# Kernel optimization log

Measured on AMD Instinct MI355X. Metric: run time of the kernel, lower is better.

Reference implementation:

```python
import jax, jax.numpy as jnp
import numpy as np

HID_GNN = 64
HID_LSTM = 128
FUTURE = 24
N_HYDRO = 32
N_METEO = 64
B, T, E = 32, 168, 384
SLOPE = 0.01  # F.leaky_relu default


def setup_inputs() -> dict:
    key = jax.random.key(0)
    ks = jax.random.split(key, 12)
    N = N_HYDRO + N_METEO
    data_meteo = jax.random.normal(ks[0], (B, T, N_METEO, 1), jnp.float32)
    data_hydro = jax.random.normal(ks[1], (B, T, N_HYDRO, 1), jnp.float32)
    edge_index = jax.random.randint(ks[2], (2, E), 0, N, dtype=jnp.int64)
    # GraphConv(1, HID_GNN): out = lin_root(x) + lin_rel(sum_j x_j) + bias
    W_root = jax.random.normal(ks[3], (HID_GNN, 1), jnp.float32) * 1.0
    W_rel = jax.random.normal(ks[4], (HID_GNN, 1), jnp.float32) * 1.0
    b_gnn = jnp.zeros((HID_GNN,), jnp.float32)
    # Per-station LSTM weights (torch gate order i,f,g,o), stacked over stations
    sih = 1.0 / np.sqrt(HID_GNN)
    shh = 1.0 / np.sqrt(HID_LSTM)
    Wih = jax.random.normal(ks[5], (N_HYDRO, 4 * HID_LSTM, HID_GNN), jnp.float32) * sih
    Whh = jax.random.normal(ks[6], (N_HYDRO, 4 * HID_LSTM, HID_LSTM), jnp.float32) * shh
    bih = jnp.zeros((N_HYDRO, 4 * HID_LSTM), jnp.float32)
    bhh = jnp.zeros((N_HYDRO, 4 * HID_LSTM), jnp.float32)
    W_lin = jax.random.normal(ks[7], (FUTURE, HID_LSTM), jnp.float32) * shh
    b_lin = jnp.zeros((FUTURE,), jnp.float32)
    return {"data_meteo": data_meteo, "data_hydro": data_hydro, "edge_index": edge_index,
            "W_root": W_root, "W_rel": W_rel, "b_gnn": b_gnn,
            "Wih": Wih, "Whh": Whh, "bih": bih, "bhh": bhh,
            "W_lin": W_lin, "b_lin": b_lin}


def _lstm_last(xs, Wih_s, Whh_s, b_s):
    # xs: [B,T,D]; one station's LSTM; returns last hidden [B,H]
    H = Whh_s.shape[1]
    h0 = jnp.zeros((xs.shape[0], H), xs.dtype)

    def step(carry, xt):
        h, c = carry
        gates = xt @ Wih_s.T + h @ Whh_s.T + b_s  # [B,4H]
        i, f, g, o = jnp.split(gates, 4, axis=-1)
        c = jax.nn.sigmoid(f) * c + jax.nn.sigmoid(i) * jnp.tanh(g)
        h = jax.nn.sigmoid(o) * jnp.tanh(c)
        return (h, c), None

    (hT, _), _ = jax.lax.scan(step, (h0, h0), jnp.swapaxes(xs, 0, 1))
    return hT


def reference(data_meteo, data_hydro, edge_index, W_root, W_rel, b_gnn,
              Wih, Whh, bih, bhh, W_lin, b_lin):
    Bn, Tn, Nh, F = data_hydro.shape
    Nm = data_meteo.shape[2]
    N = Nh + Nm
    # [B,T,N,1] -> one graph per (b,t); same edge_index in every graph
    x = jnp.concatenate([data_hydro, data_meteo], axis=2).reshape(Bn * Tn, N, F)
    src, dst = edge_index[0], edge_index[1]
    agg = jnp.zeros_like(x).at[:, dst].add(x[:, src])  # sum aggregation
    h = x @ W_root.T + agg @ W_rel.T + b_gnn          # GraphConv, [G,N,HID_GNN]
    h = jax.nn.leaky_relu(h, SLOPE)
    hydro = h.reshape(Bn, Tn, N, -1)[:, :, :Nh, :]    # [B,T,Nh,HID_GNN]
    # per-station LSTM: vmap over station axis with station-specific weights
    last = jax.vmap(_lstm_last, in_axes=(2, 0, 0, 0))(hydro, Wih, Whh, bih + bhh)  # [Nh,B,H]
    pred = last @ W_lin.T + b_lin                     # [Nh,B,FUTURE]
    pred = jnp.swapaxes(pred, 0, 1)                   # [B,Nh,FUTURE]
    return jax.nn.leaky_relu(pred, SLOPE)
```

## Files before the change

### kernel.cpp

```cpp
#include <hip/hip_runtime.h>

typedef unsigned short u16;
typedef unsigned int u32;
typedef __attribute__((ext_vector_type(8))) short short8;
typedef __attribute__((ext_vector_type(4))) float floatx4;
typedef __attribute__((ext_vector_type(4))) float float4v;

#define B_ 32
#define T_ 168
#define NH_ 32
#define NM_ 64
#define E_ 384
#define HL_ 128
#define FUT_ 24
#define SLOPE_ 0.01f
#define XP_ 80
#define HP_ 144
#define WIH_LP 72
#define WHH_LP 136
#define OVL_E (T_ * 4 * XP_)
#define XG_B 68
#define XG_T (4 * XG_B)
#define XG_W (4 * XG_T)

#define NS1_ (-1.4426950408889634f)
#define S2_ (2.8853900817779268f)

static __device__ __forceinline__ float b2f(u16 u) {
  u32 v = ((u32)u) << 16;
  return __builtin_bit_cast(float, v);
}
static __device__ __forceinline__ u16 f2bf(float f) {
  u32 x = __builtin_bit_cast(u32, f);
  u32 r = (x + 0x7fffu + ((x >> 16) & 1u)) >> 16;
  return (u16)r;
}
static __device__ __forceinline__ float fexp2(float x) { return __builtin_amdgcn_exp2f(x); }
static __device__ __forceinline__ float frcp(float x) { return __builtin_amdgcn_rcpf(x); }
static __device__ __forceinline__ float sel4(floatx4 v, int r) {
  float m0 = (r & 1) ? v[1] : v[0];
  float m1 = (r & 1) ? v[3] : v[2];
  return (r & 2) ? m1 : m0;
}
static __device__ __forceinline__ float lrelu(float x) { return fmaxf(x, SLOPE_ * x); }

__launch_bounds__(512, 2)
__global__ void fused_kernel(const float* __restrict__ dm, const float* __restrict__ dh,
                             const int* __restrict__ eidx,
                             const float* __restrict__ Wroot, const float* __restrict__ Wrel,
                             const float* __restrict__ bgnn,
                             const float* __restrict__ Wih, const float* __restrict__ Whh,
                             const float* __restrict__ bih, const float* __restrict__ bhh,
                             const float* __restrict__ Wlin, const float* __restrict__ blin,
                             float* __restrict__ out) {
  const int s = blockIdx.x & 31;
  const int bg = blockIdx.x >> 5;
  const int tid = threadIdx.x;
  const int w = tid >> 6;
  const int lane = tid & 63;
  const int cm = lane & 15;
  const int q = lane >> 4;
  const int b = cm & 3;
  const int rho = cm >> 2;

  __shared__ __align__(16) u16 ovl[OVL_E];
  __shared__ __align__(16) u16 hbuf[2 * 4 * HP_];
  __shared__ __align__(16) float xgbuf[8 * XG_W];
  __shared__ float xh_lds[4][T_];
  __shared__ float ag_lds[4][T_];
  __shared__ float wr_s[64], wv_s[64], bg_s[64];
  __shared__ int srcs[E_];
  __shared__ int nsrc, iflag;

  if (tid == 0) { nsrc = 0; iflag = 0; }
  for (int i = tid; i < 2 * 4 * HP_; i += 512) hbuf[i] = 0;
  __syncthreads();

  {
    int odd = 0;
    for (int e = tid; e < E_; e += 512) odd |= eidx[2 * e + 1];
    if (odd) atomicOr(&iflag, 1);
  }
  __syncthreads();
  const bool i32 = iflag != 0;

  for (int e = tid; e < E_; e += 512) {
    int se = i32 ? eidx[e] : eidx[2 * e];
    int de = i32 ? eidx[E_ + e] : eidx[2 * E_ + 2 * e];
    if (de == s) { int i = atomicAdd(&nsrc, 1); srcs[i] = se; }
  }
  if (tid < 64) { wr_s[tid] = Wroot[tid]; wv_s[tid] = Wrel[tid]; bg_s[tid] = bgnn[tid]; }
  for (int i = tid; i < 4 * T_; i += 512) {
    int bb = i / T_, t = i % T_;
    xh_lds[bb][t] = dh[((size_t)(bg * 4 + bb) * T_ + t) * NH_ + s];
  }
  floatx4 bias_init[4];
#pragma unroll
  for (int blk = 0; blk < 4; blk++) {
    const float scb = (blk == 2) ? S2_ : NS1_;
#pragma unroll
    for (int r = 0; r < 4; r++) {
      const int nb = blk * 128 + w * 16 + q * 4 + r;
      bias_init[blk][r] = (bih[s * 512 + nb] + bhh[s * 512 + nb]) * scb;
    }
  }
  __syncthreads();

  const int ns = nsrc;
  for (int i = tid; i < 4 * T_; i += 512) {
    int bb = i / T_, t = i % T_;
    size_t gb = (size_t)(bg * 4 + bb) * T_ + t;
    float a = 0.f;
    for (int j = 0; j < ns; j++) {
      int sr = srcs[j];
      a += (sr < NH_) ? dh[gb * NH_ + sr] : dm[gb * NM_ + (sr - NH_)];
    }
    ag_lds[bb][t] = a;
  }

  short8 Af[4][6];
  const int nl = w * 16 + cm;
  __syncthreads();
  {
    const float* g = Wih + (size_t)s * 512 * 64;
#pragma unroll
    for (int it = 0; it < 16; it++) {
      int j = tid + it * 512;
      float4v v = *(const float4v*)(g + 4 * j);
      const float sc = ((j >> 11) == 2) ? S2_ : NS1_;
      u16* dst = ovl + (j >> 4) * WIH_LP + (j & 15) * 4;
      dst[0] = f2bf(v[0] * sc); dst[1] = f2bf(v[1] * sc);
      dst[2] = f2bf(v[2] * sc); dst[3] = f2bf(v[3] * sc);
    }
  }
  __syncthreads();
#pragma unroll
  for (int blk = 0; blk < 4; blk++)
#pragma unroll
    for (int kk = 0; kk < 2; kk++)
      Af[blk][kk] = *(const short8*)(ovl + (blk * 128 + nl) * WIH_LP + kk * 32 + q * 8);
  __syncthreads();
  {
    const float* g = Whh + (size_t)s * 512 * 128;
#pragma unroll
    for (int it = 0; it < 16; it++) {
      int j = tid + it * 512;
      float4v v = *(const float4v*)(g + 4 * j);
      u16* dst = ovl + (j >> 5) * WHH_LP + (j & 31) * 4;
      dst[0] = f2bf(v[0] * NS1_); dst[1] = f2bf(v[1] * NS1_);
      dst[2] = f2bf(v[2] * NS1_); dst[3] = f2bf(v[3] * NS1_);
    }
  }
  __syncthreads();
#pragma unroll
  for (int blk = 0; blk < 2; blk++)
#pragma unroll
    for (int kk = 0; kk < 4; kk++)
      Af[blk][2 + kk] = *(const short8*)(ovl + (blk * 128 + nl) * WHH_LP + kk * 32 + q * 8);
  __syncthreads();
  {
    const float* g = Whh + ((size_t)s * 512 + 256) * 128;
#pragma unroll
    for (int it = 0; it < 16; it++) {
      int j = tid + it * 512;
      float4v v = *(const float4v*)(g + 4 * j);
      const float sc = (j < 4096) ? S2_ : NS1_;
      u16* dst = ovl + (j >> 5) * WHH_LP + (j & 31) * 4;
      dst[0] = f2bf(v[0] * sc); dst[1] = f2bf(v[1] * sc);
      dst[2] = f2bf(v[2] * sc); dst[3] = f2bf(v[3] * sc);
    }
  }
  __syncthreads();
#pragma unroll
  for (int blk = 2; blk < 4; blk++)
#pragma unroll
    for (int kk = 0; kk < 4; kk++)
      Af[blk][2 + kk] = *(const short8*)(ovl + ((blk - 2) * 128 + nl) * WHH_LP + kk * 32 + q * 8);
  __syncthreads();

  {
    const int k = tid & 63;
    const int bb = (tid >> 6) & 3;
    const int th = tid >> 8;
    const float wrk = wr_s[k], wvk = wv_s[k], bgk = bg_s[k];
    for (int i = 0; i < T_ / 2; i++) {
      const int t = th * (T_ / 2) + i;
      const float xv = xh_lds[bb][t] * wrk + ag_lds[bb][t] * wvk + bgk;
      ovl[t * (4 * XP_) + bb * XP_ + k] = f2bf(lrelu(xv));
    }
  }
  __syncthreads();

  floatx4 zvec;
  zvec[0] = 0.f; zvec[1] = 0.f; zvec[2] = 0.f; zvec[3] = 0.f;
  float* const xgw = xgbuf + w * XG_W + rho * XG_T + b * XG_B + q * 16;
  const float* const xgr = xgbuf + w * XG_W + b * XG_B + q * 16 + rho * 4;

  float c = 0.0f;
  for (int tt = 0; tt < T_ / 4; tt++) {
    {
      const int tb = tt * 4 + rho;
      short8 Bx0 = *(const short8*)(ovl + tb * (4 * XP_) + b * XP_ + q * 8);
      short8 Bx1 = *(const short8*)(ovl + tb * (4 * XP_) + b * XP_ + 32 + q * 8);
      floatx4 ax[4];
#pragma unroll
      for (int blk = 0; blk < 4; blk++) {
        ax[blk] = __builtin_amdgcn_mfma_f32_16x16x32_bf16(Af[blk][0], Bx0, bias_init[blk], 0, 0, 0);
        ax[blk] = __builtin_amdgcn_mfma_f32_16x16x32_bf16(Af[blk][1], Bx1, ax[blk], 0, 0, 0);
      }
#pragma unroll
      for (int r = 0; r < 4; r++) {
        floatx4 vv;
        vv[0] = ax[0][r]; vv[1] = ax[1][r]; vv[2] = ax[2][r]; vv[3] = ax[3][r];
        *(floatx4*)(xgw + r * 4) = vv;
      }
    }

#pragma unroll
    for (int u = 0; u < 4; u++) {
      const int p = u & 1, pn = p ^ 1;
      short8 Bh[4];
#pragma unroll
      for (int kk = 0; kk < 4; kk++)
        Bh[kk] = *(const short8*)(hbuf + p * (4 * HP_) + b * HP_ + kk * 32 + q * 8);
      const floatx4 xgv = *(const floatx4*)(xgr + u * XG_T);

      floatx4 a2 = __builtin_amdgcn_mfma_f32_16x16x32_bf16(Af[2][2], Bh[0], zvec, 0, 0, 0);
      floatx4 a0 = __builtin_amdgcn_mfma_f32_16x16x32_bf16(Af[0][2], Bh[0], zvec, 0, 0, 0);
#pragma unroll
      for (int kk = 1; kk < 4; kk++) {
        a2 = __builtin_amdgcn_mfma_f32_16x16x32_bf16(Af[2][2 + kk], Bh[kk], a2, 0, 0, 0);
        a0 = __builtin_amdgcn_mfma_f32_16x16x32_bf16(Af[0][2 + kk], Bh[kk], a0, 0, 0, 0);
      }
      const float gg = sel4(a2, rho) + xgv[2];
      const float gi = sel4(a0, rho) + xgv[0];
      const float Eg = fexp2(gg);
      const float Ei = fexp2(gi);

      floatx4 a1 = __builtin_amdgcn_mfma_f32_16x16x32_bf16(Af[1][2], Bh[0], zvec, 0, 0, 0);
      floatx4 a3 = __builtin_amdgcn_mfma_f32_16x16x32_bf16(Af[3][2], Bh[0], zvec, 0, 0, 0);
#pragma unroll
      for (int kk = 1; kk < 4; kk++) {
        a1 = __builtin_amdgcn_mfma_f32_16x16x32_bf16(Af[1][2 + kk], Bh[kk], a1, 0, 0, 0);
        a3 = __builtin_amdgcn_mfma_f32_16x16x32_bf16(Af[3][2 + kk], Bh[kk], a3, 0, 0, 0);
      }

      const float tg = 1.0f - 2.0f * frcp(1.0f + Eg);
      const float si = frcp(1.0f + Ei);
      const float gf = sel4(a1, rho) + xgv[1];
      const float go = sel4(a3, rho) + xgv[3];
      const float sf = frcp(1.0f + fexp2(gf));
      c = sf * c + si * tg;
      const float tc = 1.0f - 2.0f * frcp(1.0f + fexp2(S2_ * c));
      const float so = frcp(1.0f + fexp2(go));
      const float hh = so * tc;
      u32 pk;
      asm("v_cvt_pk_bf16_f32 %0, %1, %2" : "=v"(pk) : "v"(hh), "v"(hh));
      hbuf[pn * (4 * HP_) + b * HP_ + w * 16 + q * 4 + rho] = (u16)pk;
      __syncthreads();
    }
  }

  if (tid < 4 * FUT_) {
    const int bb = tid / FUT_;
    const int f = tid % FUT_;
    float a = blin[f];
#pragma unroll 8
    for (int k = 0; k < HL_; k++) a += b2f(hbuf[bb * HP_ + k]) * Wlin[f * HL_ + k];
    out[((size_t)(bg * 4 + bb) * NH_ + s) * FUT_ + f] = lrelu(a);
  }
}

extern "C" void kernel_launch(void* const* d_in, const int* in_sizes, int n_in,
                              void* d_out, int out_size, void* d_ws, size_t ws_size,
                              hipStream_t stream) {
  const float* dm = (const float*)d_in[0];
  const float* dh = (const float*)d_in[1];
  const int* eidx = (const int*)d_in[2];
  const float* Wroot = (const float*)d_in[3];
  const float* Wrel = (const float*)d_in[4];
  const float* bgnn = (const float*)d_in[5];
  const float* Wih = (const float*)d_in[6];
  const float* Whh = (const float*)d_in[7];
  const float* bih = (const float*)d_in[8];
  const float* bhh = (const float*)d_in[9];
  const float* Wlin = (const float*)d_in[10];
  const float* blin = (const float*)d_in[11];
  float* out = (float*)d_out;

  fused_kernel<<<256, 512, 0, stream>>>(dm, dh, eidx, Wroot, Wrel, bgnn, Wih, Whh,
                                        bih, bhh, Wlin, blin, out);
}
```

Before: 179.7 us.

## Software-pipeline input-gate MFMAs into recurrent steps with swizzled LDS staging

Computes the input projection for the next block of four timesteps inside the recurrent inner loop, one gate block per step, so those MFMAs interleave with the latency-bound recurrent chain instead of running as a separate phase. Writes results straight to LDS as floatx4 using an XOR-swizzled layout, with scalar reads, replacing the earlier register transpose. This keeps more accumulator registers live and does extra scalar LDS reads per step. The last iteration computes a redundant clamped block.

```diff
diff --git a/kernel.cpp b/kernel.cpp
--- a/kernel.cpp
+++ b/kernel.cpp
@@ -19,9 +19,6 @@
 #define WIH_LP 72
 #define WHH_LP 136
 #define OVL_E (T_ * 4 * XP_)
-#define XG_B 68
-#define XG_T (4 * XG_B)
-#define XG_W (4 * XG_T)
 
 #define NS1_ (-1.4426950408889634f)
 #define S2_ (2.8853900817779268f)
@@ -65,7 +62,7 @@
 
   __shared__ __align__(16) u16 ovl[OVL_E];
   __shared__ __align__(16) u16 hbuf[2 * 4 * HP_];
-  __shared__ __align__(16) float xgbuf[8 * XG_W];
+  __shared__ __align__(16) float xgbuf[8 * 1024];
   __shared__ float xh_lds[4][T_];
   __shared__ float ag_lds[4][T_];
   __shared__ float wr_s[64], wv_s[64], bg_s[64];
@@ -191,31 +188,37 @@
   }
   __syncthreads();
 
+  int boff[4];
+#pragma unroll
+  for (int k = 0; k < 4; k++) boff[k] = ((k ^ q) & 3) * 4;
+  float* const xgW = xgbuf + w * 1024 + rho * 256 + q * 64 + b * 16;
+  const float* const xgR = xgbuf + w * 1024 + q * 64 + b * 16 + rho;
+
   floatx4 zvec;
   zvec[0] = 0.f; zvec[1] = 0.f; zvec[2] = 0.f; zvec[3] = 0.f;
-  float* const xgw = xgbuf + w * XG_W + rho * XG_T + b * XG_B + q * 16;
-  const float* const xgr = xgbuf + w * XG_W + b * XG_B + q * 16 + rho * 4;
+
+  floatx4 pax[4];
+  {
+    short8 Bx0 = *(const short8*)(ovl + rho * (4 * XP_) + b * XP_ + q * 8);
+    short8 Bx1 = *(const short8*)(ovl + rho * (4 * XP_) + b * XP_ + 32 + q * 8);
+#pragma unroll
+    for (int k = 0; k < 4; k++) {
+      pax[k] = __builtin_amdgcn_mfma_f32_16x16x32_bf16(Af[k][0], Bx0, bias_init[k], 0, 0, 0);
+      pax[k] = __builtin_amdgcn_mfma_f32_16x16x32_bf16(Af[k][1], Bx1, pax[k], 0, 0, 0);
+    }
+  }
 
   float c = 0.0f;
   for (int tt = 0; tt < T_ / 4; tt++) {
+#pragma unroll
+    for (int k = 0; k < 4; k++) *(floatx4*)(xgW + boff[k]) = pax[k];
+
+    short8 Bn0, Bn1;
     {
-      const int tb = tt * 4 + rho;
-      short8 Bx0 = *(const short8*)(ovl + tb * (4 * XP_) + b * XP_ + q * 8);
-      short8 Bx1 = *(const short8*)(ovl + tb * (4 * XP_) + b * XP_ + 32 + q * 8);
-      floatx4 ax[4];
-#pragma unroll
-      for (int blk = 0; blk < 4; blk++) {
-        ax[blk] = __builtin_amdgcn_mfma_f32_16x16x32_bf16(Af[blk][0], Bx0, bias_init[blk], 0, 0, 0);
-        ax[blk] = __builtin_amdgcn_mfma_f32_16x16x32_bf16(Af[blk][1], Bx1, ax[blk], 0, 0, 0);
-      }
-#pragma unroll
-      for (int r = 0; r < 4; r++) {
-        floatx4 vv;
-        vv[0] = ax[0][r]; vv[1] = ax[1][r]; vv[2] = ax[2][r]; vv[3] = ax[3][r];
-        *(floatx4*)(xgw + r * 4) = vv;
-      }
-    }
-
+      const int tbn = min((tt + 1) * 4, T_ - 4) + rho;
+      Bn0 = *(const short8*)(ovl + tbn * (4 * XP_) + b * XP_ + q * 8);
+      Bn1 = *(const short8*)(ovl + tbn * (4 * XP_) + b * XP_ + 32 + q * 8);
+    }
 #pragma unroll
     for (int u = 0; u < 4; u++) {
       const int p = u & 1, pn = p ^ 1;
@@ -223,7 +226,13 @@
 #pragma unroll
       for (int kk = 0; kk < 4; kk++)
         Bh[kk] = *(const short8*)(hbuf + p * (4 * HP_) + b * HP_ + kk * 32 + q * 8);
-      const floatx4 xgv = *(const floatx4*)(xgr + u * XG_T);
+      const float xg0 = xgR[u * 256 + boff[0]];
+      const float xg1 = xgR[u * 256 + boff[1]];
+      const float xg2 = xgR[u * 256 + boff[2]];
+      const float xg3 = xgR[u * 256 + boff[3]];
+
+      pax[u] = __builtin_amdgcn_mfma_f32_16x16x32_bf16(Af[u][0], Bn0, bias_init[u], 0, 0, 0);
+      pax[u] = __builtin_amdgcn_mfma_f32_16x16x32_bf16(Af[u][1], Bn1, pax[u], 0, 0, 0);
 
       floatx4 a2 = __builtin_amdgcn_mfma_f32_16x16x32_bf16(Af[2][2], Bh[0], zvec, 0, 0, 0);
       floatx4 a0 = __builtin_amdgcn_mfma_f32_16x16x32_bf16(Af[0][2], Bh[0], zvec, 0, 0, 0);
@@ -232,8 +241,8 @@
         a2 = __builtin_amdgcn_mfma_f32_16x16x32_bf16(Af[2][2 + kk], Bh[kk], a2, 0, 0, 0);
         a0 = __builtin_amdgcn_mfma_f32_16x16x32_bf16(Af[0][2 + kk], Bh[kk], a0, 0, 0, 0);
       }
-      const float gg = sel4(a2, rho) + xgv[2];
-      const float gi = sel4(a0, rho) + xgv[0];
+      const float gg = sel4(a2, rho) + xg2;
+      const float gi = sel4(a0, rho) + xg0;
       const float Eg = fexp2(gg);
       const float Ei = fexp2(gi);
 
@@ -247,8 +256,8 @@
 
       const float tg = 1.0f - 2.0f * frcp(1.0f + Eg);
       const float si = frcp(1.0f + Ei);
-      const float gf = sel4(a1, rho) + xgv[1];
-      const float go = sel4(a3, rho) + xgv[3];
+      const float gf = sel4(a1, rho) + xg1;
+      const float go = sel4(a3, rho) + xg3;
       const float sf = frcp(1.0f + fexp2(gf));
       c = sf * c + si * tg;
       const float tc = 1.0f - 2.0f * frcp(1.0f + fexp2(S2_ * c));
```

Result: slower. 192.2 us (+6.9%).
